# Optimization experiments

Measured on AMD Instinct MI355X. Metric: run time of the kernel, lower is better.

## Reference

```python
import jax, jax.numpy as jnp
import numpy as np

B, H, D = 32, 200000, 8

def setup_inputs() -> dict:
    key = jax.random.key(0)
    k1, k2, k3, k4 = jax.random.split(key, 4)
    col = jax.random.normal(k1, (B, D), dtype=jnp.float32)
    cen = jax.random.normal(k2, (B, H, D), dtype=jnp.float32)
    prc_h = jax.random.uniform(k3, (B, H, D), dtype=jnp.float32) + 0.5  # positive precisions
    hgt_h = jax.random.uniform(k4, (B, H), dtype=jnp.float32) * 0.01    # accumulated hill heights
    kbt = jnp.ones((B,), dtype=jnp.float32)
    wdt = jnp.ones((D,), dtype=jnp.float32)
    prc = 1.0 / (wdt * wdt)                  # buffer: 1/wdt^2
    hgt = jnp.asarray(0.01, dtype=jnp.float32)  # buffer: new hill base height
    gam = jnp.asarray(10.0, dtype=jnp.float32)  # buffer: bias factor gamma
    return {"col": col, "cen": cen, "prc_h": prc_h, "hgt_h": hgt_h,
            "kbt": kbt, "prc": prc, "hgt": hgt, "gam": gam}

def reference(col, cen, prc_h, hgt_h, kbt, prc, hgt, gam):
    # gaussian_potential: V_b = sum_h hgt[b,h] * exp(-0.5 * sum_d (cen-col)^2 * prc)
    r = cen - col[:, None, :]                     # (B,H,D)
    expo = -0.5 * jnp.sum(r * r * prc_h, axis=-1)  # (B,H)
    eng = jnp.sum(hgt_h * jnp.exp(expo), axis=1)   # (B,)
    # new_gaussian_wtmtd
    det = gam * kbt - kbt                          # (B,)
    new_hgt = hgt * jnp.exp(-eng / det)            # (B,) well-tempered height
    new_prc = jnp.broadcast_to(prc[None, :], (col.shape[0], prc.shape[0]))
    # add_gaussian: append new hill along hills dim
    cen_out = jnp.concatenate([cen, col[:, None, :]], axis=1)       # (B,H+1,D)
    prc_out = jnp.concatenate([prc_h, new_prc[:, None, :]], axis=1)  # (B,H+1,D)
    hgt_out = jnp.concatenate([hgt_h, new_hgt[:, None]], axis=1)     # (B,H+1)
    return cen_out, prc_out, hgt_out
```

## Files before the change

### kernel.cpp

```cpp
#include <hip/hip_runtime.h>


#define BB 32
#define HH 200000
#define DD 8
#define BLK 256
#define IT 16
#define KB 8
#define CHUNK (BLK * IT)
#define F4B (HH * 2)

typedef float f32x4 __attribute__((ext_vector_type(4)));

__global__ __launch_bounds__(BLK) void wtmtd_main(
    const float* __restrict__ col,
    const float* __restrict__ cen,
    const float* __restrict__ prc_h,
    const float* __restrict__ hgt_h,
    float* __restrict__ cen_out,
    float* __restrict__ prc_out,
    float* __restrict__ hgt_out,
    float* __restrict__ partials)
{
    const int b = blockIdx.y;
    const int t = threadIdx.x;

    const size_t hIn  = (size_t)b * HH;
    const size_t hOut = (size_t)b * (HH + 1);

    const f32x4* cen4 = (const f32x4*)cen   + (size_t)b * F4B;
    const f32x4* prc4 = (const f32x4*)prc_h + (size_t)b * F4B;
    f32x4* co = (f32x4*)cen_out + (size_t)b * (F4B + 2);
    f32x4* po = (f32x4*)prc_out + (size_t)b * (F4B + 2);

    const f32x4* colv = (const f32x4*)(col + (size_t)b * DD);
    const f32x4 c_my  = colv[t & 1];
    const float mask0 = (t & 1) ? 0.0f : 1.0f;

    const int base  = blockIdx.x * CHUNK;
    const int hbase = base >> 1;

    #pragma unroll
    for (int i = 0; i < IT / 2; ++i) {
        const int h = hbase + i * BLK + t;
        if (h < HH) hgt_out[hOut + h] = hgt_h[hIn + h];
    }

    float local = 0.0f;
    const bool full = (base + CHUNK) <= F4B;

    if (full) {
        #pragma unroll
        for (int half = 0; half < IT / KB; ++half) {
            f32x4 v[KB], p[KB];
            #pragma unroll
            for (int j = 0; j < KB; ++j)
                v[j] = cen4[base + (half * KB + j) * BLK + t];
            #pragma unroll
            for (int j = 0; j < KB; ++j)
                p[j] = prc4[base + (half * KB + j) * BLK + t];

            #pragma unroll
            for (int j = 0; j < KB; ++j) {
                const int idx = base + (half * KB + j) * BLK + t;
                const float hh = hgt_h[hIn + (idx >> 1)];
                const f32x4 d = v[j] - c_my;
                float s = d.x*d.x*p[j].x + d.y*d.y*p[j].y
                        + d.z*d.z*p[j].z + d.w*d.w*p[j].w;
                s += __shfl_xor(s, 1);
                local += mask0 * hh * __expf(-0.5f * s);
            }

            #pragma unroll
            for (int j = 0; j < KB; ++j)
                co[base + (half * KB + j) * BLK + t] = v[j];
            #pragma unroll
            for (int j = 0; j < KB; ++j)
                po[base + (half * KB + j) * BLK + t] = p[j];
        }
    } else {
        #pragma unroll 4
        for (int i = 0; i < IT; ++i) {
            const int idx = base + i * BLK + t;
            if (idx < F4B) {
                const f32x4 v = cen4[idx];
                const f32x4 p = prc4[idx];
                const float hh = hgt_h[hIn + (idx >> 1)];

                const f32x4 d = v - c_my;
                float s = d.x*d.x*p.x + d.y*d.y*p.y + d.z*d.z*p.z + d.w*d.w*p.w;
                s += __shfl_xor(s, 1);
                local += mask0 * hh * __expf(-0.5f * s);

                co[idx] = v;
                po[idx] = p;
            }
        }
    }

    #pragma unroll
    for (int off = 32; off > 0; off >>= 1)
        local += __shfl_down(local, off);

    __shared__ float sred[BLK / 64];
    const int lane = t & 63;
    const int wv   = t >> 6;
    if (lane == 0) sred[wv] = local;
    __syncthreads();
    if (t == 0) {
        float s = 0.0f;
        #pragma unroll
        for (int i = 0; i < BLK / 64; ++i) s += sred[i];
        partials[(size_t)b * gridDim.x + blockIdx.x] = s;
    }
}

__global__ __launch_bounds__(64) void wtmtd_fin(
    const float* __restrict__ partials, int nblk,
    const float* __restrict__ col,
    const float* __restrict__ kbt,
    const float* __restrict__ prc,
    const float* __restrict__ hgt,
    const float* __restrict__ gam,
    float* __restrict__ cen_out,
    float* __restrict__ prc_out,
    float* __restrict__ hgt_out)
{
    const int b = blockIdx.x;

    float s = 0.0f;
    for (int i = threadIdx.x; i < nblk; i += 64)
        s += partials[(size_t)b * nblk + i];
    #pragma unroll
    for (int off = 32; off > 0; off >>= 1)
        s += __shfl_down(s, off);
    s = __shfl(s, 0);

    const float det = kbt[b] * (gam[0] - 1.0f);
    const float new_hgt = hgt[0] * expf(-s / det);

    const size_t outBase = (size_t)b * (HH + 1);
    if (threadIdx.x < DD) {
        cen_out[(outBase + HH) * DD + threadIdx.x] = col[(size_t)b * DD + threadIdx.x];
        prc_out[(outBase + HH) * DD + threadIdx.x] = prc[threadIdx.x];
    }
    if (threadIdx.x == 0)
        hgt_out[outBase + HH] = new_hgt;
}

extern "C" void kernel_launch(void* const* d_in, const int* in_sizes, int n_in,
                              void* d_out, int out_size, void* d_ws, size_t ws_size,
                              hipStream_t stream) {
    const float* col   = (const float*)d_in[0];
    const float* cen   = (const float*)d_in[1];
    const float* prc_h = (const float*)d_in[2];
    const float* hgt_h = (const float*)d_in[3];
    const float* kbt   = (const float*)d_in[4];
    const float* prc   = (const float*)d_in[5];
    const float* hgt   = (const float*)d_in[6];
    const float* gam   = (const float*)d_in[7];

    float* cen_out = (float*)d_out;
    float* prc_out = cen_out + (size_t)BB * (HH + 1) * DD;
    float* hgt_out = prc_out + (size_t)BB * (HH + 1) * DD;

    float* partials = (float*)d_ws;

    const int nblkx = (F4B + CHUNK - 1) / CHUNK;
    dim3 grid(nblkx, BB);

    wtmtd_main<<<grid, BLK, 0, stream>>>(col, cen, prc_h, hgt_h,
                                         cen_out, prc_out, hgt_out, partials);
    wtmtd_fin<<<BB, 64, 0, stream>>>(partials, nblkx, col, kbt, prc, hgt, gam,
                                     cen_out, prc_out, hgt_out);
}
```

Before: 168.8 us.

## Double-buffer burst loads in main kernel and double chunk per block

Each block now processes four bursts of eight float4 loads per array instead of two. A ping-pong register buffer keeps the next burst's loads in flight while the current burst is computed and stored. The goal is more memory-level parallelism to hide load latency in this bandwidth-bound copy-and-reduce kernel. In exchange the kernel needs twice the vector registers, which may lower occupancy, and the grid has half as many blocks.

```diff
diff --git a/kernel.cpp b/kernel.cpp
--- a/kernel.cpp
+++ b/kernel.cpp
@@ -5,12 +5,54 @@
 #define HH 200000
 #define DD 8
 #define BLK 256
-#define IT 16
 #define KB 8
+#define NH 4
+#define IT (KB * NH)
 #define CHUNK (BLK * IT)
 #define F4B (HH * 2)
 
 typedef float f32x4 __attribute__((ext_vector_type(4)));
+
+__device__ __forceinline__ void load_burst(
+    const f32x4* __restrict__ cen4, const f32x4* __restrict__ prc4,
+    int base, int k, int t, f32x4 (&v)[KB], f32x4 (&p)[KB])
+{
+    #pragma unroll
+    for (int j = 0; j < KB; ++j)
+        v[j] = cen4[base + (k * KB + j) * BLK + t];
+    #pragma unroll
+    for (int j = 0; j < KB; ++j)
+        p[j] = prc4[base + (k * KB + j) * BLK + t];
+}
+
+__device__ __forceinline__ void compute_burst(
+    const f32x4 (&v)[KB], const f32x4 (&p)[KB],
+    const float* __restrict__ hgt_h, size_t hIn,
+    int base, int k, int t, f32x4 c_my, float mask0, float& local)
+{
+    #pragma unroll
+    for (int j = 0; j < KB; ++j) {
+        const int idx = base + (k * KB + j) * BLK + t;
+        const float hh = hgt_h[hIn + (idx >> 1)];
+        const f32x4 d = v[j] - c_my;
+        float s = d.x*d.x*p[j].x + d.y*d.y*p[j].y
+                + d.z*d.z*p[j].z + d.w*d.w*p[j].w;
+        s += __shfl_xor(s, 1);
+        local += mask0 * hh * __expf(-0.5f * s);
+    }
+}
+
+__device__ __forceinline__ void store_burst(
+    f32x4* __restrict__ co, f32x4* __restrict__ po,
+    int base, int k, int t, const f32x4 (&v)[KB], const f32x4 (&p)[KB])
+{
+    #pragma unroll
+    for (int j = 0; j < KB; ++j)
+        co[base + (k * KB + j) * BLK + t] = v[j];
+    #pragma unroll
+    for (int j = 0; j < KB; ++j)
+        po[base + (k * KB + j) * BLK + t] = p[j];
+}
 
 __global__ __launch_bounds__(BLK) void wtmtd_main(
     const float* __restrict__ col,
@@ -50,34 +92,22 @@
     const bool full = (base + CHUNK) <= F4B;
 
     if (full) {
-        #pragma unroll
-        for (int half = 0; half < IT / KB; ++half) {
-            f32x4 v[KB], p[KB];
-            #pragma unroll
-            for (int j = 0; j < KB; ++j)
-                v[j] = cen4[base + (half * KB + j) * BLK + t];
-            #pragma unroll
-            for (int j = 0; j < KB; ++j)
-                p[j] = prc4[base + (half * KB + j) * BLK + t];
-
-            #pragma unroll
-            for (int j = 0; j < KB; ++j) {
-                const int idx = base + (half * KB + j) * BLK + t;
-                const float hh = hgt_h[hIn + (idx >> 1)];
-                const f32x4 d = v[j] - c_my;
-                float s = d.x*d.x*p[j].x + d.y*d.y*p[j].y
-                        + d.z*d.z*p[j].z + d.w*d.w*p[j].w;
-                s += __shfl_xor(s, 1);
-                local += mask0 * hh * __expf(-0.5f * s);
-            }
-
-            #pragma unroll
-            for (int j = 0; j < KB; ++j)
-                co[base + (half * KB + j) * BLK + t] = v[j];
-            #pragma unroll
-            for (int j = 0; j < KB; ++j)
-                po[base + (half * KB + j) * BLK + t] = p[j];
-        }
+        f32x4 vA[KB], pA[KB], vB[KB], pB[KB];
+        load_burst(cen4, prc4, base, 0, t, vA, pA);
+        load_burst(cen4, prc4, base, 1, t, vB, pB);
+
+        compute_burst(vA, pA, hgt_h, hIn, base, 0, t, c_my, mask0, local);
+        store_burst(co, po, base, 0, t, vA, pA);
+        load_burst(cen4, prc4, base, 2, t, vA, pA);
+
+        compute_burst(vB, pB, hgt_h, hIn, base, 1, t, c_my, mask0, local);
+        store_burst(co, po, base, 1, t, vB, pB);
+        load_burst(cen4, prc4, base, 3, t, vB, pB);
+
+        compute_burst(vA, pA, hgt_h, hIn, base, 2, t, c_my, mask0, local);
+        store_burst(co, po, base, 2, t, vA, pA);
+        compute_burst(vB, pB, hgt_h, hIn, base, 3, t, c_my, mask0, local);
+        store_burst(co, po, base, 3, t, vB, pB);
     } else {
         #pragma unroll 4
         for (int i = 0; i < IT; ++i) {
```

After: 192.3 us. 1.14x slower.
